# Kernel optimization log

Measured on AMD Instinct MI355X. Metric: run time of the kernel, lower is better.

## Reference

```python
import jax, jax.numpy as jnp
import numpy as np

NUM_HEADS = 16
HEAD_DIM = 128


def rotate_half(x):
    x1, x2 = jnp.split(x, 2, axis=-1)
    return jnp.concatenate((-x2, x1), axis=-1)


def setup_inputs() -> dict:
    key = jax.random.key(0)
    ks = jax.random.split(key, 6)
    B, S, H = 2, 2048, 2048
    hidden_states = jax.random.normal(ks[0], (B, S, H), dtype=jnp.float32)
    # RoPE cos/sin tables (HF-style: half-dim freqs duplicated)
    inv_freq = 1.0 / (10000.0 ** (jnp.arange(0, HEAD_DIM, 2, dtype=jnp.float32) / HEAD_DIM))
    t = jnp.arange(S, dtype=jnp.float32)
    freqs = jnp.outer(t, inv_freq)                      # [S, HEAD_DIM/2]
    emb = jnp.concatenate((freqs, freqs), axis=-1)      # [S, HEAD_DIM]
    cos = jnp.cos(emb)
    sin = jnp.sin(emb)
    attention_mask = jnp.zeros((1, 1, S, S), dtype=jnp.float32)
    scale = 0.02
    Wq = jax.random.normal(ks[1], (H, H), dtype=jnp.float32) * scale
    Wk = jax.random.normal(ks[2], (H, H), dtype=jnp.float32) * scale
    Wv = jax.random.normal(ks[3], (H, H), dtype=jnp.float32) * scale
    Wo = jax.random.normal(ks[4], (H, H), dtype=jnp.float32) * scale
    return {"hidden_states": hidden_states, "cos": cos, "sin": sin,
            "attention_mask": attention_mask, "Wq": Wq, "Wk": Wk, "Wv": Wv, "Wo": Wo}


def reference(hidden_states, cos, sin, attention_mask, Wq, Wk, Wv, Wo):
    B, S, H = hidden_states.shape
    nh, hd = NUM_HEADS, HEAD_DIM
    # nn.Linear(bias=False): x @ W.T
    q = hidden_states @ Wq.T
    k = hidden_states @ Wk.T
    v = hidden_states @ Wv.T
    # [B, nh, S, hd]
    q = q.reshape(B, S, nh, hd).transpose(0, 2, 1, 3)
    k = k.reshape(B, S, nh, hd).transpose(0, 2, 1, 3)
    v = v.reshape(B, S, nh, hd).transpose(0, 2, 1, 3)
    # RoPE
    c = cos[None, None, :, :]
    s = sin[None, None, :, :]
    q = q * c + rotate_half(q) * s
    k = k * c + rotate_half(k) * s
    scores = jnp.einsum("bhqd,bhkd->bhqk", q, k) / jnp.sqrt(jnp.float32(hd))
    scores = scores + attention_mask
    attn = jax.nn.softmax(scores, axis=-1)
    out = jnp.einsum("bhqk,bhkd->bhqd", attn, v)
    out = out.transpose(0, 2, 1, 3).reshape(B, S, H)
    return out @ Wo.T
```

## Files before the change

### kernel.cpp

```cpp
#include <hip/hip_runtime.h>
#include <stdint.h>

typedef __bf16 bf16;
typedef __attribute__((ext_vector_type(4))) __bf16 bf16x4;
typedef __attribute__((ext_vector_type(8))) __bf16 bf16x8;
typedef __attribute__((ext_vector_type(4))) float f32x4;

__device__ __forceinline__ void gl2lds16(const void* g, void* l) {
  __builtin_amdgcn_global_load_lds(
      (__attribute__((address_space(1))) void*)(uintptr_t)g,
      (__attribute__((address_space(3))) void*)(uint32_t)(uintptr_t)l,
      16, 0, 0);
}

__global__ __launch_bounds__(256) void cast_to_bf16(const float* __restrict__ x,
                                                    bf16* __restrict__ y, int n4) {
  int i = blockIdx.x * 256 + threadIdx.x;
  if (i >= n4) return;
  float4 v = ((const float4*)x)[i];
  bf16x4 o;
  o[0] = (bf16)v.x; o[1] = (bf16)v.y; o[2] = (bf16)v.z; o[3] = (bf16)v.w;
  ((bf16x4*)y)[i] = o;
}

__global__ __launch_bounds__(256) void cast_w4(const float* __restrict__ s0,
                                               const float* __restrict__ s1,
                                               const float* __restrict__ s2,
                                               const float* __restrict__ s3,
                                               bf16* __restrict__ d0, bf16* __restrict__ d1,
                                               bf16* __restrict__ d2, bf16* __restrict__ d3) {
  int i = blockIdx.x * 256 + threadIdx.x;
  int wsel = i >> 20;
  int j = i & 1048575;
  const float* s = wsel == 0 ? s0 : wsel == 1 ? s1 : wsel == 2 ? s2 : s3;
  bf16* d = wsel == 0 ? d0 : wsel == 1 ? d1 : wsel == 2 ? d2 : d3;
  float4 v = ((const float4*)s)[j];
  bf16x4 o;
  o[0] = (bf16)v.x; o[1] = (bf16)v.y; o[2] = (bf16)v.z; o[3] = (bf16)v.w;
  ((bf16x4*)d)[j] = o;
}

template <typename OutT>
__global__ __launch_bounds__(256) void gemm_bt(const bf16* __restrict__ A,
                                               const bf16* __restrict__ B,
                                               OutT* __restrict__ C,
                                               int M, int N, int K) {
  __shared__ bf16 As[128 * 64];
  __shared__ bf16 Bs[128 * 64];
  const int t = threadIdx.x;
  const int w = t >> 6;
  const int lane = t & 63;
  const int quad = lane >> 4;
  const int m16 = lane & 15;
  const int wr = w >> 1;
  const int wc = w & 1;
  const size_t rowA0 = (size_t)blockIdx.y * 128;
  const size_t rowB0 = (size_t)blockIdx.x * 128;

  f32x4 acc[4][4];
#pragma unroll
  for (int i = 0; i < 4; ++i)
#pragma unroll
    for (int j = 0; j < 4; ++j) {
      f32x4 z = {0.f, 0.f, 0.f, 0.f};
      acc[i][j] = z;
    }

  const int srow = lane >> 3;
  const int sg = (lane & 7) ^ (srow & 7);

#pragma unroll 1
  for (int kt = 0; kt < K; kt += 64) {
    __syncthreads();
#pragma unroll
    for (int i = 0; i < 4; ++i) {
      const int ch = w * 4 + i;
      const int r = ch * 8 + srow;
      gl2lds16(A + (rowA0 + r) * (size_t)K + kt + sg * 8, &As[ch * 512]);
      gl2lds16(B + (rowB0 + r) * (size_t)K + kt + sg * 8, &Bs[ch * 512]);
    }
    __syncthreads();
#pragma unroll
    for (int ks = 0; ks < 2; ++ks) {
      bf16x8 af[4], bfr[4];
      const int g = ks * 4 + quad;
      const int gs = (g ^ (m16 & 7)) * 8;
#pragma unroll
      for (int i = 0; i < 4; ++i) {
        af[i]  = *(const bf16x8*)&As[(wr * 64 + i * 16 + m16) * 64 + gs];
        bfr[i] = *(const bf16x8*)&Bs[(wc * 64 + i * 16 + m16) * 64 + gs];
      }
#pragma unroll
      for (int i = 0; i < 4; ++i)
#pragma unroll
        for (int j = 0; j < 4; ++j)
          acc[i][j] = __builtin_amdgcn_mfma_f32_16x16x32_bf16(af[i], bfr[j], acc[i][j], 0, 0, 0);
    }
  }

#pragma unroll
  for (int i = 0; i < 4; ++i)
#pragma unroll
    for (int j = 0; j < 4; ++j)
#pragma unroll
      for (int r = 0; r < 4; ++r) {
        size_t row = rowA0 + wr * 64 + i * 16 + quad * 4 + r;
        size_t col = rowB0 + wc * 64 + j * 16 + m16;
        float v = acc[i][j][r];
        if constexpr (__is_same(OutT, float)) C[row * N + col] = v;
        else                                  C[row * N + col] = (bf16)v;
      }
}

__global__ __launch_bounds__(256) void rope_kernel(bf16* __restrict__ X,
                                                   const float* __restrict__ cosp,
                                                   const float* __restrict__ sinp) {
  int tid = blockIdx.x * 256 + threadIdx.x;
  int d = tid & 63;
  int hh = (tid >> 6) & 31;
  int tok = tid >> 11;
  if (tok >= 4096) return;
  int s = tok & 2047;
  const float sl2e = 0.088388347648318447f * 1.4426950408889634f;
  float qs = hh < 16 ? sl2e : 1.0f;
  size_t base = (size_t)tok * 4096 + hh * 128 + d;
  float c = cosp[s * 128 + d];
  float sn = sinp[s * 128 + d];
  float x1 = (float)X[base];
  float x2 = (float)X[base + 64];
  X[base]      = (bf16)((x1 * c - x2 * sn) * qs);
  X[base + 64] = (bf16)((x2 * c + x1 * sn) * qs);
}

__global__ __launch_bounds__(256) void flash_attn(const bf16* __restrict__ Qg,
                                                  const bf16* __restrict__ Kg,
                                                  const bf16* __restrict__ Vt,
                                                  bf16* __restrict__ O) {
  __shared__ bf16 Ks[64 * 128];
  __shared__ bf16 Vs[128 * 64];
  __shared__ bf16 Ps[4][32 * 72];

  const int t = threadIdx.x;
  const int w = t >> 6;
  const int lane = t & 63;
  const int quad = lane >> 4;
  const int m16 = lane & 15;
  const int qt = blockIdx.x;
  const int bh = blockIdx.y;
  const int b = bh >> 4;
  const int h = bh & 15;

  bf16x8 qf[2][4];
#pragma unroll
  for (int half = 0; half < 2; ++half) {
    const int qrow = qt * 128 + w * 32 + half * 16 + m16;
    const bf16* qp = Qg + (size_t)(b * 2048 + qrow) * 4096 + h * 128 + quad * 8;
#pragma unroll
    for (int ks = 0; ks < 4; ++ks) qf[half][ks] = *(const bf16x8*)(qp + ks * 32);
  }

  const int krl = lane >> 4;
  const int vrl = lane >> 3;
  const int vg = (lane & 7) ^ (vrl & 7);

  f32x4 o[2][8];
#pragma unroll
  for (int half = 0; half < 2; ++half)
#pragma unroll
    for (int i = 0; i < 8; ++i) { f32x4 z = {0.f, 0.f, 0.f, 0.f}; o[half][i] = z; }
  float lsum[2][4] = {{0.f, 0.f, 0.f, 0.f}, {0.f, 0.f, 0.f, 0.f}};

#pragma unroll 1
  for (int kt = 0; kt < 32; ++kt) {
    __syncthreads();
#pragma unroll
    for (int i = 0; i < 4; ++i) {
      const int c = w * 4 + i;
      const int krow = c * 4 + krl;
      const int kgg = (lane & 15) ^ (krow & 15);
      gl2lds16(Kg + (size_t)(b * 2048 + kt * 64 + krow) * 4096 + h * 128 + kgg * 8,
               &Ks[c * 512]);
      const int vrow = c * 8 + vrl;
      gl2lds16(Vt + (size_t)(h * 128 + vrow) * 4096 + b * 2048 + kt * 64 + vg * 8,
               &Vs[c * 512]);
    }
    __syncthreads();

    f32x4 sc[2][4];
#pragma unroll
    for (int half = 0; half < 2; ++half)
#pragma unroll
      for (int nb = 0; nb < 4; ++nb) {
        f32x4 z = {0.f, 0.f, 0.f, 0.f};
        sc[half][nb] = z;
      }
#pragma unroll
    for (int nb = 0; nb < 4; ++nb)
#pragma unroll
      for (int ks = 0; ks < 4; ++ks) {
        bf16x8 kf = *(const bf16x8*)&Ks[(nb * 16 + m16) * 128 + ((ks * 4 + quad) ^ m16) * 8];
        sc[0][nb] = __builtin_amdgcn_mfma_f32_16x16x32_bf16(qf[0][ks], kf, sc[0][nb], 0, 0, 0);
        sc[1][nb] = __builtin_amdgcn_mfma_f32_16x16x32_bf16(qf[1][ks], kf, sc[1][nb], 0, 0, 0);
      }

#pragma unroll
    for (int half = 0; half < 2; ++half)
#pragma unroll
      for (int nb = 0; nb < 4; ++nb)
#pragma unroll
        for (int r = 0; r < 4; ++r) {
          float p = __builtin_amdgcn_exp2f(sc[half][nb][r]);
          lsum[half][r] += p;
          Ps[w][(half * 16 + quad * 4 + r) * 72 + nb * 16 + m16] = (bf16)p;
        }

    bf16x8 pf[2][2];
#pragma unroll
    for (int half = 0; half < 2; ++half)
#pragma unroll
      for (int ks = 0; ks < 2; ++ks)
        pf[half][ks] = *(const bf16x8*)&Ps[w][(half * 16 + m16) * 72 + ks * 32 + quad * 8];

#pragma unroll
    for (int db = 0; db < 8; ++db)
#pragma unroll
      for (int ks = 0; ks < 2; ++ks) {
        bf16x8 vf = *(const bf16x8*)&Vs[(db * 16 + m16) * 64 + ((ks * 4 + quad) ^ (m16 & 7)) * 8];
        o[0][db] = __builtin_amdgcn_mfma_f32_16x16x32_bf16(pf[0][ks], vf, o[0][db], 0, 0, 0);
        o[1][db] = __builtin_amdgcn_mfma_f32_16x16x32_bf16(pf[1][ks], vf, o[1][db], 0, 0, 0);
      }
  }

#pragma unroll
  for (int off = 1; off < 16; off <<= 1)
#pragma unroll
    for (int half = 0; half < 2; ++half)
#pragma unroll
      for (int r = 0; r < 4; ++r) lsum[half][r] += __shfl_xor(lsum[half][r], off);

  float inv[2][4];
#pragma unroll
  for (int half = 0; half < 2; ++half)
#pragma unroll
    for (int r = 0; r < 4; ++r) inv[half][r] = 1.0f / lsum[half][r];

#pragma unroll
  for (int half = 0; half < 2; ++half)
#pragma unroll
    for (int db = 0; db < 8; ++db)
#pragma unroll
      for (int r = 0; r < 4; ++r) {
        int row = qt * 128 + w * 32 + half * 16 + quad * 4 + r;
        O[(size_t)(b * 2048 + row) * 2048 + h * 128 + db * 16 + m16] =
            (bf16)(o[half][db][r] * inv[half][r]);
      }
}

extern "C" void kernel_launch(void* const* d_in, const int* in_sizes, int n_in,
                              void* d_out, int out_size, void* d_ws, size_t ws_size,
                              hipStream_t stream) {
  const float* hs   = (const float*)d_in[0];
  const float* cosp = (const float*)d_in[1];
  const float* sinp = (const float*)d_in[2];
  const float* Wq   = (const float*)d_in[4];
  const float* Wk   = (const float*)d_in[5];
  const float* Wv   = (const float*)d_in[6];
  const float* Wo   = (const float*)d_in[7];
  float* out = (float*)d_out;

  char* ws = (char*)d_ws;
  bf16* Xb   = (bf16*)(ws);
  bf16* Wqkb = (bf16*)(ws + 16777216);
  bf16* Wvb  = (bf16*)(ws + 33554432);
  bf16* Wob  = (bf16*)(ws + 41943040);
  bf16* QKb  = (bf16*)(ws + 50331648);
  bf16* Vtb  = (bf16*)(ws + 83886080);
  bf16* Ob   = Xb;

  cast_to_bf16<<<8192, 256, 0, stream>>>(hs, Xb, 2097152);
  cast_w4<<<16384, 256, 0, stream>>>(Wq, Wk, Wv, Wo,
                                     Wqkb, Wqkb + 4194304, Wvb, Wob);

  gemm_bt<bf16><<<dim3(32, 32), 256, 0, stream>>>(Xb, Wqkb, QKb, 4096, 4096, 2048);
  gemm_bt<bf16><<<dim3(32, 16), 256, 0, stream>>>(Wvb, Xb, Vtb, 2048, 4096, 2048);

  rope_kernel<<<32768, 256, 0, stream>>>(QKb, cosp, sinp);

  flash_attn<<<dim3(16, 32), 256, 0, stream>>>(QKb, QKb + 2048, Vtb, Ob);

  gemm_bt<float><<<dim3(16, 32), 256, 0, stream>>>(Ob, Wob, out, 4096, 2048, 2048);
}
```

Before: 492.7 us.

## Double-buffer K/V tiles and keep P in registers via transposed MFMA

The flash attention kernel now double-buffers K and V tiles in LDS, issuing the next tile's global-to-LDS loads before computing on the current one, which drops one barrier per iteration. It computes S transposed (K as the A operand) so the exp'd probabilities already sit in the B-operand layout of a 16x16x16 MFMA. This removes the per-wave P shared-memory round trip. The output is written as packed bf16x4 stores and the row-sum reduction shrinks to two shuffles. It doubles LDS use (64KB), which may lower occupancy, and the PV product now uses twice as many smaller MFMAs.

```diff
diff --git a/kernel.cpp b/kernel.cpp
--- a/kernel.cpp
+++ b/kernel.cpp
@@ -5,12 +5,22 @@
 typedef __attribute__((ext_vector_type(4))) __bf16 bf16x4;
 typedef __attribute__((ext_vector_type(8))) __bf16 bf16x8;
 typedef __attribute__((ext_vector_type(4))) float f32x4;
+typedef __attribute__((ext_vector_type(4))) short short4v;
 
 __device__ __forceinline__ void gl2lds16(const void* g, void* l) {
   __builtin_amdgcn_global_load_lds(
       (__attribute__((address_space(1))) void*)(uintptr_t)g,
       (__attribute__((address_space(3))) void*)(uint32_t)(uintptr_t)l,
       16, 0, 0);
+}
+
+__device__ __forceinline__ f32x4 mfma_16x16x16(bf16x4 a, bf16x4 b, f32x4 c) {
+#if defined(__HIP_DEVICE_COMPILE__)
+  return __builtin_amdgcn_mfma_f32_16x16x16bf16_1k(
+      __builtin_bit_cast(short4v, a), __builtin_bit_cast(short4v, b), c, 0, 0, 0);
+#else
+  return c;
+#endif
 }
 
 __global__ __launch_bounds__(256) void cast_to_bf16(const float* __restrict__ x,
@@ -136,9 +146,8 @@
                                                   const bf16* __restrict__ Kg,
                                                   const bf16* __restrict__ Vt,
                                                   bf16* __restrict__ O) {
-  __shared__ bf16 Ks[64 * 128];
-  __shared__ bf16 Vs[128 * 64];
-  __shared__ bf16 Ps[4][32 * 72];
+  __shared__ bf16 Ks[2][64 * 128];
+  __shared__ bf16 Vs[2][128 * 64];
 
   const int t = threadIdx.x;
   const int w = t >> 6;
@@ -163,97 +172,94 @@
   const int vrl = lane >> 3;
   const int vg = (lane & 7) ^ (vrl & 7);
 
-  f32x4 o[2][8];
-#pragma unroll
-  for (int half = 0; half < 2; ++half)
-#pragma unroll
-    for (int i = 0; i < 8; ++i) { f32x4 z = {0.f, 0.f, 0.f, 0.f}; o[half][i] = z; }
-  float lsum[2][4] = {{0.f, 0.f, 0.f, 0.f}, {0.f, 0.f, 0.f, 0.f}};
-
-#pragma unroll 1
-  for (int kt = 0; kt < 32; ++kt) {
-    __syncthreads();
+  auto stage = [&](int buf, int kt) {
 #pragma unroll
     for (int i = 0; i < 4; ++i) {
       const int c = w * 4 + i;
       const int krow = c * 4 + krl;
       const int kgg = (lane & 15) ^ (krow & 15);
       gl2lds16(Kg + (size_t)(b * 2048 + kt * 64 + krow) * 4096 + h * 128 + kgg * 8,
-               &Ks[c * 512]);
+               &Ks[buf][c * 512]);
       const int vrow = c * 8 + vrl;
       gl2lds16(Vt + (size_t)(h * 128 + vrow) * 4096 + b * 2048 + kt * 64 + vg * 8,
-               &Vs[c * 512]);
-    }
+               &Vs[buf][c * 512]);
+    }
+  };
+
+  f32x4 o[2][8];
+#pragma unroll
+  for (int half = 0; half < 2; ++half)
+#pragma unroll
+    for (int i = 0; i < 8; ++i) { f32x4 z = {0.f, 0.f, 0.f, 0.f}; o[half][i] = z; }
+  float lsum[2] = {0.f, 0.f};
+
+  stage(0, 0);
+
+#pragma unroll 1
+  for (int kt = 0; kt < 32; ++kt) {
+    const int cur = kt & 1;
     __syncthreads();
-
-    f32x4 sc[2][4];
+    if (kt < 31) stage(cur ^ 1, kt + 1);
+
+    f32x4 st[2][4];
 #pragma unroll
     for (int half = 0; half < 2; ++half)
 #pragma unroll
       for (int nb = 0; nb < 4; ++nb) {
         f32x4 z = {0.f, 0.f, 0.f, 0.f};
-        sc[half][nb] = z;
+        st[half][nb] = z;
       }
 #pragma unroll
     for (int nb = 0; nb < 4; ++nb)
 #pragma unroll
       for (int ks = 0; ks < 4; ++ks) {
-        bf16x8 kf = *(const bf16x8*)&Ks[(nb * 16 + m16) * 128 + ((ks * 4 + quad) ^ m16) * 8];
-        sc[0][nb] = __builtin_amdgcn_mfma_f32_16x16x32_bf16(qf[0][ks], kf, sc[0][nb], 0, 0, 0);
-        sc[1][nb] = __builtin_amdgcn_mfma_f32_16x16x32_bf16(qf[1][ks], kf, sc[1][nb], 0, 0, 0);
-      }
-
+        bf16x8 kf = *(const bf16x8*)&Ks[cur][(nb * 16 + m16) * 128 + ((ks * 4 + quad) ^ m16) * 8];
+        st[0][nb] = __builtin_amdgcn_mfma_f32_16x16x32_bf16(kf, qf[0][ks], st[0][nb], 0, 0, 0);
+        st[1][nb] = __builtin_amdgcn_mfma_f32_16x16x32_bf16(kf, qf[1][ks], st[1][nb], 0, 0, 0);
+      }
+
+    bf16x4 pA[2][4];
 #pragma unroll
     for (int half = 0; half < 2; ++half)
 #pragma unroll
       for (int nb = 0; nb < 4; ++nb)
 #pragma unroll
         for (int r = 0; r < 4; ++r) {
-          float p = __builtin_amdgcn_exp2f(sc[half][nb][r]);
-          lsum[half][r] += p;
-          Ps[w][(half * 16 + quad * 4 + r) * 72 + nb * 16 + m16] = (bf16)p;
+          float p = __builtin_amdgcn_exp2f(st[half][nb][r]);
+          lsum[half] += p;
+          pA[half][nb][r] = (bf16)p;
         }
 
-    bf16x8 pf[2][2];
-#pragma unroll
-    for (int half = 0; half < 2; ++half)
-#pragma unroll
-      for (int ks = 0; ks < 2; ++ks)
-        pf[half][ks] = *(const bf16x8*)&Ps[w][(half * 16 + m16) * 72 + ks * 32 + quad * 8];
-
 #pragma unroll
     for (int db = 0; db < 8; ++db)
 #pragma unroll
-      for (int ks = 0; ks < 2; ++ks) {
-        bf16x8 vf = *(const bf16x8*)&Vs[(db * 16 + m16) * 64 + ((ks * 4 + quad) ^ (m16 & 7)) * 8];
-        o[0][db] = __builtin_amdgcn_mfma_f32_16x16x32_bf16(pf[0][ks], vf, o[0][db], 0, 0, 0);
-        o[1][db] = __builtin_amdgcn_mfma_f32_16x16x32_bf16(pf[1][ks], vf, o[1][db], 0, 0, 0);
-      }
-  }
-
-#pragma unroll
-  for (int off = 1; off < 16; off <<= 1)
-#pragma unroll
-    for (int half = 0; half < 2; ++half)
-#pragma unroll
-      for (int r = 0; r < 4; ++r) lsum[half][r] += __shfl_xor(lsum[half][r], off);
-
-  float inv[2][4];
-#pragma unroll
-  for (int half = 0; half < 2; ++half)
-#pragma unroll
-    for (int r = 0; r < 4; ++r) inv[half][r] = 1.0f / lsum[half][r];
-
-#pragma unroll
-  for (int half = 0; half < 2; ++half)
-#pragma unroll
-    for (int db = 0; db < 8; ++db)
-#pragma unroll
-      for (int r = 0; r < 4; ++r) {
-        int row = qt * 128 + w * 32 + half * 16 + quad * 4 + r;
-        O[(size_t)(b * 2048 + row) * 2048 + h * 128 + db * 16 + m16] =
-            (bf16)(o[half][db][r] * inv[half][r]);
-      }
+      for (int nb = 0; nb < 4; ++nb) {
+        bf16x4 vB = *(const bf16x4*)&Vs[cur][(db * 16 + m16) * 64 +
+            (((nb * 2 + (quad >> 1)) ^ (m16 & 7)) * 8 + (quad & 1) * 4)];
+        o[0][db] = mfma_16x16x16(vB, pA[0][nb], o[0][db]);
+        o[1][db] = mfma_16x16x16(vB, pA[1][nb], o[1][db]);
+      }
+  }
+
+#pragma unroll
+  for (int half = 0; half < 2; ++half) {
+    lsum[half] += __shfl_xor(lsum[half], 16);
+    lsum[half] += __shfl_xor(lsum[half], 32);
+  }
+  float inv[2] = {1.0f / lsum[0], 1.0f / lsum[1]};
+
+#pragma unroll
+  for (int half = 0; half < 2; ++half) {
+    const int row = qt * 128 + w * 32 + half * 16 + m16;
+    bf16* op = O + (size_t)(b * 2048 + row) * 2048 + h * 128 + quad * 4;
+#pragma unroll
+    for (int db = 0; db < 8; ++db) {
+      bf16x4 ov;
+#pragma unroll
+      for (int r = 0; r < 4; ++r) ov[r] = (bf16)(o[half][db][r] * inv[half]);
+      *(bf16x4*)(op + db * 16) = ov;
+    }
+  }
 }
 
 extern "C" void kernel_launch(void* const* d_in, const int* in_sizes, int n_in,
```

Measured after the change: 423.4 us. 14.1% less time.
